# Performance work log

Hardware: AMD Instinct MI355X
Metric: run time of the kernel (lower is better)

The kernel has to match this reference:

```python
import jax, jax.numpy as jnp
import numpy as np

NEG_SLOPE = 0.2  # init arg negative_slope


def setup_inputs() -> dict:
    key = jax.random.key(0)
    k1, k2, k3, k4 = jax.random.split(key, 4)
    N, E, D_IN, D_OUT = 8192, 262144, 128, 128
    h = jax.random.normal(k1, (N, D_IN), dtype=jnp.float32)
    edge_index = jax.random.randint(k2, (2, E), 0, N, dtype=jnp.int64)
    # nn.Linear(in, out, bias=False) weight: [out, in]
    W = jax.random.normal(k3, (D_OUT, D_IN), dtype=jnp.float32) * (1.0 / np.sqrt(D_IN))
    # att parameter: [2*out, 1], xavier-uniform-ish scale
    lim = np.sqrt(6.0 / (2 * D_OUT + 1)) * 1.414
    att = jax.random.uniform(k4, (2 * D_OUT, 1), dtype=jnp.float32, minval=-lim, maxval=lim)
    return {"h": h, "edge_index": edge_index, "W": W, "att": att}


def reference(h, edge_index, W, att):
    # h: [N, d_in], edge_index: [2, E], W: [d_out, d_in], att: [2*d_out, 1]
    h_trans = h @ W.T                                  # [N, d_out]
    row, col = edge_index[0], edge_index[1]
    e = jnp.concatenate([h_trans[row], h_trans[col]], axis=1)  # [E, 2*d_out]
    edge_e = jnp.squeeze(e @ att, axis=-1)             # [E]
    edge_e = jnp.where(edge_e >= 0, edge_e, NEG_SLOPE * edge_e)  # leaky_relu
    N = h.shape[0]
    attention = jnp.zeros((N, N), dtype=h_trans.dtype).at[row, col].set(edge_e)
    attention = (attention + attention.T) * 0.5        # symmetrize
    fill_value = edge_e.max()                          # .item() -> constant (no grad)
    diag = jnp.arange(N)
    attention = attention.at[diag, diag].set(fill_value)
    attention = jax.nn.softmax(attention, axis=1)      # row softmax over dense NxN
    h_prime = attention @ h_trans                      # [N, d_out]
    h_prime = jax.nn.elu(h_prime)                      # concat=True -> ELU
    # F.dropout in eval mode is identity
    return h_prime, attention
```

## Files before the change

kernel.cpp:

```cpp
#include <hip/hip_runtime.h>
#include <stdint.h>

#define NN 8192
#define EE 262144
#define DD 128
#define NEGS 0.2f
#define HBITS 20

__device__ __forceinline__ unsigned f2ord(float f){
  unsigned u = __float_as_uint(f);
  return (u & 0x80000000u) ? ~u : (u | 0x80000000u);
}
__device__ __forceinline__ float ord2f(unsigned u){
  return __uint_as_float((u & 0x80000000u) ? (u & 0x7fffffffu) : ~u);
}
__device__ __forceinline__ unsigned hmix(int key){
  unsigned h = (unsigned)key * 2654435761u;
  h ^= h >> 15;
  return h;
}

__global__ void k_hashclear(int* hkeys, int* hvals){
  int i = blockIdx.x*256 + threadIdx.x;
  int4 m1 = {-1,-1,-1,-1};
  ((int4*)hkeys)[i] = m1;
  ((int4*)hvals)[i] = m1;
}

__global__ void k_init(int* cnt, int* cursor, float* T, unsigned* fillmax){
  int i = blockIdx.x*256 + threadIdx.x;
  if(i < NN){ cnt[i] = 0; cursor[i] = 0; }
  if(i < DD) T[i] = 0.f;
  if(i == 0) *fillmax = 0x007FFFFFu;
}

__global__ void k_wt(const float* __restrict__ W, float* __restrict__ wt){
  int idx = blockIdx.x*256 + threadIdx.x;
  int c = idx >> 7, k = idx & 127;
  wt[k*DD + c] = W[idx];
}

__global__ __launch_bounds__(256) void k_gemm(const float* __restrict__ h,
                                              const float* __restrict__ wt,
                                              float* __restrict__ ht){
  __shared__ float wl[64*DD];
  __shared__ float hl[16][132];
  int t = threadIdx.x;
  int row0 = blockIdx.x * 16;
  #pragma unroll
  for(int u=0;u<2;u++){
    int f4 = u*256 + t;
    int r = f4 >> 5, k4 = f4 & 31;
    float4 v = ((const float4*)(h + (size_t)(row0+r)*DD))[k4];
    *((float4*)&hl[r][k4*4]) = v;
  }
  int r  = t >> 4;
  int c0 = (t & 15) * 8;
  float acc[8];
  #pragma unroll
  for(int s=0;s<8;s++) acc[s]=0.f;
  for(int p=0;p<2;p++){
    __syncthreads();
    const float4* wsrc = (const float4*)(wt + p*64*DD);
    float4* wd = (float4*)wl;
    #pragma unroll
    for(int u=0;u<8;u++) wd[u*256+t] = wsrc[u*256+t];
    __syncthreads();
    #pragma unroll 4
    for(int kk=0;kk<64;kk++){
      float hv = hl[r][p*64+kk];
      const float* wrow = &wl[kk*DD + c0];
      #pragma unroll
      for(int s=0;s<8;s++) acc[s] += hv * wrow[s];
    }
  }
  float4 o0 = {acc[0],acc[1],acc[2],acc[3]};
  float4 o1 = {acc[4],acc[5],acc[6],acc[7]};
  float4* o = (float4*)(ht + (size_t)(row0+r)*DD + c0);
  o[0]=o0; o[1]=o1;
}

__global__ void k_colsum(const float* __restrict__ ht, float* T){
  __shared__ float part[256];
  int t = threadIdx.x; int c = t & 127; int half = t >> 7;
  float s = 0.f;
  int r0 = blockIdx.x*128 + half*64;
  for(int r=r0; r<r0+64; r++) s += ht[(size_t)r*DD + c];
  part[t] = s; __syncthreads();
  if(half==0) atomicAdd(&T[c], part[t] + part[t+128]);
}

__global__ void k_a(const float* __restrict__ ht, const float* __restrict__ att,
                    float* a1, float* a2){
  int lane = threadIdx.x & 63;
  int i = blockIdx.x*4 + (threadIdx.x >> 6);
  const float* hr = ht + (size_t)i*DD;
  float x1 = hr[lane]*att[lane]    + hr[lane+64]*att[lane+64];
  float x2 = hr[lane]*att[DD+lane] + hr[lane+64]*att[DD+lane+64];
  #pragma unroll
  for(int o=32;o>0;o>>=1){ x1 += __shfl_down(x1,o); x2 += __shfl_down(x2,o); }
  if(lane==0){ a1[i]=x1; a2[i]=x2; }
}

__global__ void k_edge(const int* __restrict__ ei, const float* __restrict__ a1,
                       const float* __restrict__ a2, float* __restrict__ val,
                       unsigned* fillmax, int* hkeys, int* hvals, int hmask){
  int k = blockIdx.x*256 + threadIdx.x;
  int r = ei[k], c = ei[EE + k];
  float e = a1[r] + a2[c];
  e = e >= 0.f ? e : NEGS*e;
  val[k] = e;
  float wm = e;
  #pragma unroll
  for(int o=32;o>0;o>>=1) wm = fmaxf(wm, __shfl_down(wm,o));
  __shared__ float sm[4];
  if((threadIdx.x & 63)==0) sm[threadIdx.x>>6] = wm;
  __syncthreads();
  if(threadIdx.x==0){
    float bm = fmaxf(fmaxf(sm[0],sm[1]), fmaxf(sm[2],sm[3]));
    atomicMax(fillmax, f2ord(bm));
  }
  if(r != c){
    int key = r*NN + c;
    unsigned slot = hmix(key) & hmask;
    while(true){
      int prev = atomicCAS(&hkeys[slot], -1, key);
      if(prev == -1 || prev == key){ atomicMax(&hvals[slot], k); break; }
      slot = (slot + 1) & hmask;
    }
  }
}

__global__ void k_count(const int* __restrict__ hkeys, int* cnt, int hmask){
  int s = blockIdx.x*256 + threadIdx.x;
  int key = hkeys[s];
  if(key < 0) return;
  int i = key >> 13, j = key & (NN-1);
  int rkey = j*NN + i;
  unsigned slot = hmix(rkey) & hmask;
  int found = 0;
  while(true){
    int kk = hkeys[slot];
    if(kk == rkey){ found = 1; break; }
    if(kk == -1) break;
    slot = (slot + 1) & hmask;
  }
  atomicAdd(&cnt[i], 1);
  if(!found) atomicAdd(&cnt[j], 1);
}

__global__ void k_scan(const int* __restrict__ cnt, int* rowstart){
  __shared__ int part[1024];
  int t = threadIdx.x;
  int loc[8]; int s = 0;
  #pragma unroll
  for(int u=0;u<8;u++){ loc[u]=s; s += cnt[t*8+u]; }
  part[t] = s; __syncthreads();
  for(int o=1;o<1024;o<<=1){
    int add = (t>=o) ? part[t-o] : 0;
    __syncthreads();
    part[t] += add;
    __syncthreads();
  }
  int pre = part[t] - s;
  #pragma unroll
  for(int u=0;u<8;u++) rowstart[t*8+u] = pre + loc[u];
  if(t==1023) rowstart[NN] = part[1023];
}

__global__ void k_fill(const int* __restrict__ hkeys, const int* __restrict__ hvals,
                       const float* __restrict__ val, const int* __restrict__ rowstart,
                       int* cursor, int* __restrict__ ecol, float* __restrict__ eval,
                       int hmask){
  int s = blockIdx.x*256 + threadIdx.x;
  int key = hkeys[s];
  if(key < 0) return;
  int i = key >> 13, j = key & (NN-1);
  int kwin = hvals[s];
  int rkey = j*NN + i;
  unsigned slot = hmix(rkey) & hmask;
  int krev = -1;
  while(true){
    int kk = hkeys[slot];
    if(kk == rkey){ krev = hvals[slot]; break; }
    if(kk == -1) break;
    slot = (slot + 1) & hmask;
  }
  float a = 0.5f * (val[kwin] + (krev >= 0 ? val[krev] : 0.f));
  int p = rowstart[i] + atomicAdd(&cursor[i], 1);
  ecol[p] = j; eval[p] = a;
  if(krev < 0){
    int q = rowstart[j] + atomicAdd(&cursor[j], 1);
    ecol[q] = i; eval[q] = a;
  }
}

__global__ __launch_bounds__(256) void k_row(const float* __restrict__ ht,
    const float* __restrict__ T, const int* __restrict__ rowst,
    const int* __restrict__ cnt, const int* __restrict__ ecol,
    const float* __restrict__ eval, const unsigned* __restrict__ fillmax,
    float* m_, float* inv_, float* z_, float* dg_, float* __restrict__ hprime){
  int lane = threadIdx.x & 63;
  int i = blockIdx.x*4 + (threadIdx.x >> 6);
  float fill = ord2f(*fillmax);
  int st = rowst[i], n = cnt[i];
  float mx = -INFINITY;
  for(int e=lane; e<n; e+=64) mx = fmaxf(mx, eval[st+e]);
  #pragma unroll
  for(int o=32;o>0;o>>=1) mx = fmaxf(mx, __shfl_xor(mx, o));
  float m = fmaxf(fill, mx);
  if(n < NN-1) m = fmaxf(m, 0.f);
  float dsum = 0.f;
  for(int e=lane; e<n; e+=64) dsum += __expf(eval[st+e]-m);
  #pragma unroll
  for(int o=32;o>0;o>>=1) dsum += __shfl_xor(dsum, o);
  float ez = __expf(-m);
  float ef = __expf(fill-m);
  float denom = dsum + ef + (float)(NN-1-n)*ez;
  float invd = 1.f/denom;
  if(lane==0){ m_[i]=m; inv_[i]=invd; z_[i]=ez*invd; dg_[i]=ef*invd; }
  const float* hti = ht + (size_t)i*DD;
  float acc0 = ez*T[lane]    + (ef-ez)*hti[lane];
  float acc1 = ez*T[lane+64] + (ef-ez)*hti[lane+64];
  for(int e=0;e<n;e++){
    int j = ecol[st+e];
    float w = __expf(eval[st+e]-m) - ez;
    const float* htj = ht + (size_t)j*DD;
    acc0 += w*htj[lane];
    acc1 += w*htj[lane+64];
  }
  acc0 *= invd; acc1 *= invd;
  acc0 = acc0 > 0.f ? acc0 : expm1f(acc0);
  acc1 = acc1 > 0.f ? acc1 : expm1f(acc1);
  hprime[(size_t)i*DD + lane]      = acc0;
  hprime[(size_t)i*DD + lane + 64] = acc1;
}

__global__ __launch_bounds__(256) void k_dense(const int* __restrict__ rowst,
    const int* __restrict__ cnt, const int* __restrict__ ecol,
    const float* __restrict__ eval, const float* __restrict__ m_,
    const float* __restrict__ inv_, const float* __restrict__ z_,
    const float* __restrict__ dg_, float* __restrict__ attn){
  __shared__ float rowbuf[NN];
  int i = blockIdx.x, t = threadIdx.x;
  float z = z_[i], m = m_[i], inv = inv_[i];
  float4 zv = {z,z,z,z};
  float4* rb4 = (float4*)rowbuf;
  #pragma unroll
  for(int u=0;u<8;u++) rb4[u*256+t] = zv;
  __syncthreads();
  int st = rowst[i], n = cnt[i];
  for(int e=t; e<n; e+=256)
    rowbuf[ecol[st+e]] = __expf(eval[st+e]-m)*inv;
  if(t==0) rowbuf[i] = dg_[i];
  __syncthreads();
  float4* o = (float4*)(attn + (size_t)i*NN);
  #pragma unroll
  for(int u=0;u<8;u++) o[u*256+t] = rb4[u*256+t];
}

extern "C" void kernel_launch(void* const* d_in, const int* in_sizes, int n_in,
                              void* d_out, int out_size, void* d_ws, size_t ws_size,
                              hipStream_t stream){
  const float* h   = (const float*)d_in[0];
  const int*   ei  = (const int*)d_in[1];
  const float* W   = (const float*)d_in[2];
  const float* att = (const float*)d_in[3];
  float* out = (float*)d_out;
  float* hprime = out;
  float* attn   = out + (size_t)NN*DD;

  const int hsize = 1 << HBITS, hmask = hsize - 1;
  int*   hkeys = (int*)attn;
  int*   hvals = hkeys + hsize;
  float* ht    = (float*)(hvals + hsize);
  float* val   = ht + (size_t)NN*DD;
  float* wt    = val + EE;
  float* a1    = wt + DD*DD;
  float* a2    = a1 + NN;

  char* ws = (char*)d_ws;
  size_t off = 0;
  auto alloc = [&](size_t bytes)->char*{
    char* p = ws + off;
    off = (off + bytes + 15) & ~(size_t)15;
    return p;
  };
  int*   ecol   = (int*)alloc((size_t)2*EE*4);
  float* eval   = (float*)alloc((size_t)2*EE*4);
  float* T      = (float*)alloc((size_t)DD*4);
  float* m_     = (float*)alloc((size_t)NN*4);
  float* inv_   = (float*)alloc((size_t)NN*4);
  float* z_     = (float*)alloc((size_t)NN*4);
  float* dg_    = (float*)alloc((size_t)NN*4);
  int*   cnt    = (int*)alloc((size_t)NN*4);
  int*   rowst  = (int*)alloc((size_t)(NN+1)*4);
  int*   cursor = (int*)alloc((size_t)NN*4);
  unsigned* fillmax = (unsigned*)alloc(16);

  k_hashclear<<<hsize/(256*4), 256, 0, stream>>>(hkeys, hvals);
  k_init  <<<32, 256, 0, stream>>>(cnt, cursor, T, fillmax);
  k_wt    <<<64, 256, 0, stream>>>(W, wt);
  k_gemm  <<<NN/16, 256, 0, stream>>>(h, wt, ht);
  k_colsum<<<64, 256, 0, stream>>>(ht, T);
  k_a     <<<NN/4, 256, 0, stream>>>(ht, att, a1, a2);
  k_edge  <<<EE/256, 256, 0, stream>>>(ei, a1, a2, val, fillmax, hkeys, hvals, hmask);
  k_count <<<hsize/256, 256, 0, stream>>>(hkeys, cnt, hmask);
  k_scan  <<<1, 1024, 0, stream>>>(cnt, rowst);
  k_fill  <<<hsize/256, 256, 0, stream>>>(hkeys, hvals, val, rowst, cursor, ecol, eval, hmask);
  k_row   <<<NN/4, 256, 0, stream>>>(ht, T, rowst, cnt, ecol, eval, fillmax, m_, inv_, z_, dg_, hprime);
  k_dense <<<NN, 256, 0, stream>>>(rowst, cnt, ecol, eval, m_, inv_, z_, dg_, attn);
}
```

Baseline: 229.0 us.

## Fuse setup, stats and output kernels; replace CSR build with fixed-capacity buckets

Merges the init/clear/transpose kernels into one setup kernel and the colsum and attention-score kernels into one stats kernel. Replaces the count, scan and fill CSR construction with per-row fixed-capacity buckets filled directly via atomics. Fuses the row-aggregation and dense attention-write kernels into a single per-row kernel using nontemporal stores, and remaps GEMM threads with float4 shared loads. This removes several launches and a pass over the hash table, but rows with more than the bucket capacity of neighbors would be silently truncated.

```diff
diff --git a/kernel.cpp b/kernel.cpp
--- a/kernel.cpp
+++ b/kernel.cpp
@@ -6,6 +6,11 @@
 #define DD 128
 #define NEGS 0.2f
 #define HBITS 20
+#define HSIZE (1<<HBITS)
+#define HMASK (HSIZE-1)
+#define BCAP 192
+
+typedef float f32x4 __attribute__((ext_vector_type(4)));
 
 __device__ __forceinline__ unsigned f2ord(float f){
   unsigned u = __float_as_uint(f);
@@ -20,24 +25,20 @@
   return h;
 }
 
-__global__ void k_hashclear(int* hkeys, int* hvals){
-  int i = blockIdx.x*256 + threadIdx.x;
+__global__ void k_setup(int* hkeys, int* hvals, int* cnt, float* T,
+                        unsigned* fillmax, const float* __restrict__ W,
+                        float* __restrict__ wt){
+  int gid = blockIdx.x*256 + threadIdx.x;
   int4 m1 = {-1,-1,-1,-1};
-  ((int4*)hkeys)[i] = m1;
-  ((int4*)hvals)[i] = m1;
-}
-
-__global__ void k_init(int* cnt, int* cursor, float* T, unsigned* fillmax){
-  int i = blockIdx.x*256 + threadIdx.x;
-  if(i < NN){ cnt[i] = 0; cursor[i] = 0; }
-  if(i < DD) T[i] = 0.f;
-  if(i == 0) *fillmax = 0x007FFFFFu;
-}
-
-__global__ void k_wt(const float* __restrict__ W, float* __restrict__ wt){
-  int idx = blockIdx.x*256 + threadIdx.x;
-  int c = idx >> 7, k = idx & 127;
-  wt[k*DD + c] = W[idx];
+  if(gid < HSIZE/4)            ((int4*)hkeys)[gid] = m1;
+  else if(gid < HSIZE/2)       ((int4*)hvals)[gid - HSIZE/4] = m1;
+  if(gid < NN/4)               ((int4*)cnt)[gid] = int4{0,0,0,0};
+  if(gid < DD/4)               ((float4*)T)[gid] = float4{0.f,0.f,0.f,0.f};
+  if(gid == 0)                 *fillmax = 0x007FFFFFu;
+  if(gid < DD*DD){
+    int c = gid >> 7, k = gid & 127;
+    wt[k*DD + c] = W[gid];
+  }
 }
 
 __global__ __launch_bounds__(256) void k_gemm(const float* __restrict__ h,
@@ -54,8 +55,8 @@
     float4 v = ((const float4*)(h + (size_t)(row0+r)*DD))[k4];
     *((float4*)&hl[r][k4*4]) = v;
   }
-  int r  = t >> 4;
-  int c0 = (t & 15) * 8;
+  int r  = t & 15;
+  int c0 = (t >> 4) * 8;
   float acc[8];
   #pragma unroll
   for(int s=0;s<8;s++) acc[s]=0.f;
@@ -66,45 +67,46 @@
     #pragma unroll
     for(int u=0;u<8;u++) wd[u*256+t] = wsrc[u*256+t];
     __syncthreads();
-    #pragma unroll 4
+    #pragma unroll 2
     for(int kk=0;kk<64;kk++){
       float hv = hl[r][p*64+kk];
-      const float* wrow = &wl[kk*DD + c0];
-      #pragma unroll
-      for(int s=0;s<8;s++) acc[s] += hv * wrow[s];
-    }
-  }
-  float4 o0 = {acc[0],acc[1],acc[2],acc[3]};
-  float4 o1 = {acc[4],acc[5],acc[6],acc[7]};
+      const float4* wr4 = (const float4*)&wl[kk*DD + c0];
+      float4 w0 = wr4[0], w1 = wr4[1];
+      acc[0] += hv*w0.x; acc[1] += hv*w0.y; acc[2] += hv*w0.z; acc[3] += hv*w0.w;
+      acc[4] += hv*w1.x; acc[5] += hv*w1.y; acc[6] += hv*w1.z; acc[7] += hv*w1.w;
+    }
+  }
   float4* o = (float4*)(ht + (size_t)(row0+r)*DD + c0);
-  o[0]=o0; o[1]=o1;
-}
-
-__global__ void k_colsum(const float* __restrict__ ht, float* T){
-  __shared__ float part[256];
-  int t = threadIdx.x; int c = t & 127; int half = t >> 7;
-  float s = 0.f;
-  int r0 = blockIdx.x*128 + half*64;
-  for(int r=r0; r<r0+64; r++) s += ht[(size_t)r*DD + c];
-  part[t] = s; __syncthreads();
-  if(half==0) atomicAdd(&T[c], part[t] + part[t+128]);
-}
-
-__global__ void k_a(const float* __restrict__ ht, const float* __restrict__ att,
-                    float* a1, float* a2){
-  int lane = threadIdx.x & 63;
-  int i = blockIdx.x*4 + (threadIdx.x >> 6);
+  o[0] = float4{acc[0],acc[1],acc[2],acc[3]};
+  o[1] = float4{acc[4],acc[5],acc[6],acc[7]};
+}
+
+__global__ __launch_bounds__(256) void k_stats(const float* __restrict__ ht,
+    const float* __restrict__ att, float* T, float* a1, float* a2){
+  int t = threadIdx.x, b = blockIdx.x;
+  int lane = t & 63;
+  int i = b*4 + (t >> 6);
   const float* hr = ht + (size_t)i*DD;
-  float x1 = hr[lane]*att[lane]    + hr[lane+64]*att[lane+64];
-  float x2 = hr[lane]*att[DD+lane] + hr[lane+64]*att[DD+lane+64];
+  float h0 = hr[lane], h1 = hr[lane+64];
+  float x1 = h0*att[lane]    + h1*att[lane+64];
+  float x2 = h0*att[DD+lane] + h1*att[DD+lane+64];
   #pragma unroll
   for(int o=32;o>0;o>>=1){ x1 += __shfl_down(x1,o); x2 += __shfl_down(x2,o); }
   if(lane==0){ a1[i]=x1; a2[i]=x2; }
+  if(b < 64){
+    __shared__ float part[256];
+    int c = t & 127, half = t >> 7;
+    float s = 0.f;
+    int r0 = b*128 + half*64;
+    for(int rr=r0; rr<r0+64; rr++) s += ht[(size_t)rr*DD + c];
+    part[t] = s; __syncthreads();
+    if(half==0) atomicAdd(&T[c], part[t] + part[t+128]);
+  }
 }
 
 __global__ void k_edge(const int* __restrict__ ei, const float* __restrict__ a1,
                        const float* __restrict__ a2, float* __restrict__ val,
-                       unsigned* fillmax, int* hkeys, int* hvals, int hmask){
+                       unsigned* fillmax, int* hkeys, int* hvals){
   int k = blockIdx.x*256 + threadIdx.x;
   int r = ei[k], c = ei[EE + k];
   float e = a1[r] + a2[c];
@@ -121,142 +123,108 @@
     atomicMax(fillmax, f2ord(bm));
   }
   if(r != c){
-    int key = r*NN + c;
-    unsigned slot = hmix(key) & hmask;
+    int key = (r<<13) | c;
+    unsigned slot = hmix(key) & HMASK;
     while(true){
       int prev = atomicCAS(&hkeys[slot], -1, key);
       if(prev == -1 || prev == key){ atomicMax(&hvals[slot], k); break; }
-      slot = (slot + 1) & hmask;
-    }
-  }
-}
-
-__global__ void k_count(const int* __restrict__ hkeys, int* cnt, int hmask){
-  int s = blockIdx.x*256 + threadIdx.x;
-  int key = hkeys[s];
-  if(key < 0) return;
-  int i = key >> 13, j = key & (NN-1);
-  int rkey = j*NN + i;
-  unsigned slot = hmix(rkey) & hmask;
-  int found = 0;
-  while(true){
-    int kk = hkeys[slot];
-    if(kk == rkey){ found = 1; break; }
-    if(kk == -1) break;
-    slot = (slot + 1) & hmask;
-  }
-  atomicAdd(&cnt[i], 1);
-  if(!found) atomicAdd(&cnt[j], 1);
-}
-
-__global__ void k_scan(const int* __restrict__ cnt, int* rowstart){
-  __shared__ int part[1024];
-  int t = threadIdx.x;
-  int loc[8]; int s = 0;
-  #pragma unroll
-  for(int u=0;u<8;u++){ loc[u]=s; s += cnt[t*8+u]; }
-  part[t] = s; __syncthreads();
-  for(int o=1;o<1024;o<<=1){
-    int add = (t>=o) ? part[t-o] : 0;
-    __syncthreads();
-    part[t] += add;
-    __syncthreads();
-  }
-  int pre = part[t] - s;
-  #pragma unroll
-  for(int u=0;u<8;u++) rowstart[t*8+u] = pre + loc[u];
-  if(t==1023) rowstart[NN] = part[1023];
+      slot = (slot + 1) & HMASK;
+    }
+  }
 }
 
 __global__ void k_fill(const int* __restrict__ hkeys, const int* __restrict__ hvals,
-                       const float* __restrict__ val, const int* __restrict__ rowstart,
-                       int* cursor, int* __restrict__ ecol, float* __restrict__ eval,
-                       int hmask){
-  int s = blockIdx.x*256 + threadIdx.x;
-  int key = hkeys[s];
-  if(key < 0) return;
-  int i = key >> 13, j = key & (NN-1);
-  int kwin = hvals[s];
-  int rkey = j*NN + i;
-  unsigned slot = hmix(rkey) & hmask;
-  int krev = -1;
-  while(true){
-    int kk = hkeys[slot];
-    if(kk == rkey){ krev = hvals[slot]; break; }
-    if(kk == -1) break;
-    slot = (slot + 1) & hmask;
-  }
-  float a = 0.5f * (val[kwin] + (krev >= 0 ? val[krev] : 0.f));
-  int p = rowstart[i] + atomicAdd(&cursor[i], 1);
-  ecol[p] = j; eval[p] = a;
-  if(krev < 0){
-    int q = rowstart[j] + atomicAdd(&cursor[j], 1);
-    ecol[q] = i; eval[q] = a;
-  }
-}
-
-__global__ __launch_bounds__(256) void k_row(const float* __restrict__ ht,
-    const float* __restrict__ T, const int* __restrict__ rowst,
-    const int* __restrict__ cnt, const int* __restrict__ ecol,
-    const float* __restrict__ eval, const unsigned* __restrict__ fillmax,
-    float* m_, float* inv_, float* z_, float* dg_, float* __restrict__ hprime){
-  int lane = threadIdx.x & 63;
-  int i = blockIdx.x*4 + (threadIdx.x >> 6);
+                       const float* __restrict__ val, int* cnt,
+                       int2* __restrict__ bucket){
+  int base = (blockIdx.x*256 + threadIdx.x) * 2;
+  #pragma unroll
+  for(int u=0;u<2;u++){
+    int s = base + u;
+    int key = hkeys[s];
+    if(key < 0) continue;
+    int i = key >> 13, j = key & (NN-1);
+    int kwin = hvals[s];
+    int rkey = (j<<13) | i;
+    unsigned slot = hmix(rkey) & HMASK;
+    int krev = -1;
+    while(true){
+      int kk = hkeys[slot];
+      if(kk == rkey){ krev = hvals[slot]; break; }
+      if(kk == -1) break;
+      slot = (slot + 1) & HMASK;
+    }
+    float a = 0.5f * (val[kwin] + (krev >= 0 ? val[krev] : 0.f));
+    int p = atomicAdd(&cnt[i], 1);
+    if(p < BCAP) bucket[(size_t)i*BCAP + p] = int2{j, __float_as_int(a)};
+    if(krev < 0){
+      int q = atomicAdd(&cnt[j], 1);
+      if(q < BCAP) bucket[(size_t)j*BCAP + q] = int2{i, __float_as_int(a)};
+    }
+  }
+}
+
+__global__ __launch_bounds__(256) void k_out(const float* __restrict__ ht,
+    const float* __restrict__ T, const int* __restrict__ cnt,
+    const int2* __restrict__ bucket, const unsigned* __restrict__ fillmax,
+    float* __restrict__ hprime, float* __restrict__ attn){
+  __shared__ float rowbuf[NN];
+  __shared__ float red[16];
+  __shared__ float hacc[2][DD];
+  int i = blockIdx.x, t = threadIdx.x;
+  int lane = t & 63, w = t >> 6;
   float fill = ord2f(*fillmax);
-  int st = rowst[i], n = cnt[i];
+  int n = min(cnt[i], BCAP);
+  const int2* brow = bucket + (size_t)i*BCAP;
   float mx = -INFINITY;
-  for(int e=lane; e<n; e+=64) mx = fmaxf(mx, eval[st+e]);
-  #pragma unroll
-  for(int o=32;o>0;o>>=1) mx = fmaxf(mx, __shfl_xor(mx, o));
+  for(int e=t; e<n; e+=256) mx = fmaxf(mx, __int_as_float(brow[e].y));
+  #pragma unroll
+  for(int o=32;o>0;o>>=1) mx = fmaxf(mx, __shfl_xor(mx,o));
+  if(lane==0) red[w] = mx;
+  __syncthreads();
+  mx = fmaxf(fmaxf(red[0],red[1]), fmaxf(red[2],red[3]));
   float m = fmaxf(fill, mx);
-  if(n < NN-1) m = fmaxf(m, 0.f);
-  float dsum = 0.f;
-  for(int e=lane; e<n; e+=64) dsum += __expf(eval[st+e]-m);
-  #pragma unroll
-  for(int o=32;o>0;o>>=1) dsum += __shfl_xor(dsum, o);
+  m = fmaxf(m, 0.f);
+  float ds = 0.f;
+  for(int e=t; e<n; e+=256) ds += __expf(__int_as_float(brow[e].y) - m);
+  #pragma unroll
+  for(int o=32;o>0;o>>=1) ds += __shfl_xor(ds,o);
+  if(lane==0) red[8+w] = ds;
+  __syncthreads();
+  ds = red[8]+red[9]+red[10]+red[11];
   float ez = __expf(-m);
-  float ef = __expf(fill-m);
-  float denom = dsum + ef + (float)(NN-1-n)*ez;
+  float ef = __expf(fill - m);
+  float denom = ds + ef + (float)(NN-1-n)*ez;
   float invd = 1.f/denom;
-  if(lane==0){ m_[i]=m; inv_[i]=invd; z_[i]=ez*invd; dg_[i]=ef*invd; }
-  const float* hti = ht + (size_t)i*DD;
-  float acc0 = ez*T[lane]    + (ef-ez)*hti[lane];
-  float acc1 = ez*T[lane+64] + (ef-ez)*hti[lane+64];
-  for(int e=0;e<n;e++){
-    int j = ecol[st+e];
-    float w = __expf(eval[st+e]-m) - ez;
-    const float* htj = ht + (size_t)j*DD;
-    acc0 += w*htj[lane];
-    acc1 += w*htj[lane+64];
-  }
-  acc0 *= invd; acc1 *= invd;
-  acc0 = acc0 > 0.f ? acc0 : expm1f(acc0);
-  acc1 = acc1 > 0.f ? acc1 : expm1f(acc1);
-  hprime[(size_t)i*DD + lane]      = acc0;
-  hprime[(size_t)i*DD + lane + 64] = acc1;
-}
-
-__global__ __launch_bounds__(256) void k_dense(const int* __restrict__ rowst,
-    const int* __restrict__ cnt, const int* __restrict__ ecol,
-    const float* __restrict__ eval, const float* __restrict__ m_,
-    const float* __restrict__ inv_, const float* __restrict__ z_,
-    const float* __restrict__ dg_, float* __restrict__ attn){
-  __shared__ float rowbuf[NN];
-  int i = blockIdx.x, t = threadIdx.x;
-  float z = z_[i], m = m_[i], inv = inv_[i];
+  int d = t & 127, half = t >> 7;
+  float acc = (half==0) ? (ez*T[d] + (ef-ez)*ht[(size_t)i*DD+d]) : 0.f;
+  for(int e=half; e<n; e+=2){
+    int2 be = brow[e];
+    float wgt = __expf(__int_as_float(be.y) - m) - ez;
+    acc += wgt * ht[(size_t)be.x*DD + d];
+  }
+  hacc[half][d] = acc;
+  __syncthreads();
+  if(t < DD){
+    float s = (hacc[0][t] + hacc[1][t]) * invd;
+    s = s > 0.f ? s : expm1f(s);
+    hprime[(size_t)i*DD + t] = s;
+  }
+  float z = ez*invd;
   float4 zv = {z,z,z,z};
   float4* rb4 = (float4*)rowbuf;
   #pragma unroll
   for(int u=0;u<8;u++) rb4[u*256+t] = zv;
   __syncthreads();
-  int st = rowst[i], n = cnt[i];
-  for(int e=t; e<n; e+=256)
-    rowbuf[ecol[st+e]] = __expf(eval[st+e]-m)*inv;
-  if(t==0) rowbuf[i] = dg_[i];
-  __syncthreads();
-  float4* o = (float4*)(attn + (size_t)i*NN);
-  #pragma unroll
-  for(int u=0;u<8;u++) o[u*256+t] = rb4[u*256+t];
+  for(int e=t; e<n; e+=256){
+    int2 be = brow[e];
+    rowbuf[be.x] = __expf(__int_as_float(be.y)-m)*invd;
+  }
+  if(t==0) rowbuf[i] = ef*invd;
+  __syncthreads();
+  const f32x4* rbn = (const f32x4*)rowbuf;
+  f32x4* o = (f32x4*)(attn + (size_t)i*NN);
+  #pragma unroll
+  for(int u=0;u<8;u++) __builtin_nontemporal_store(rbn[u*256+t], o + u*256+t);
 }
 
 extern "C" void kernel_launch(void* const* d_in, const int* in_sizes, int n_in,
@@ -270,44 +238,30 @@
   float* hprime = out;
   float* attn   = out + (size_t)NN*DD;
 
-  const int hsize = 1 << HBITS, hmask = hsize - 1;
   int*   hkeys = (int*)attn;
-  int*   hvals = hkeys + hsize;
-  float* ht    = (float*)(hvals + hsize);
-  float* val   = ht + (size_t)NN*DD;
-  float* wt    = val + EE;
-  float* a1    = wt + DD*DD;
+  int*   hvals = hkeys + HSIZE;
+  float* val   = (float*)(hvals + HSIZE);
+  float* a1    = val + EE;
   float* a2    = a1 + NN;
 
   char* ws = (char*)d_ws;
   size_t off = 0;
   auto alloc = [&](size_t bytes)->char*{
     char* p = ws + off;
-    off = (off + bytes + 15) & ~(size_t)15;
+    off = (off + bytes + 255) & ~(size_t)255;
     return p;
   };
-  int*   ecol   = (int*)alloc((size_t)2*EE*4);
-  float* eval   = (float*)alloc((size_t)2*EE*4);
-  float* T      = (float*)alloc((size_t)DD*4);
-  float* m_     = (float*)alloc((size_t)NN*4);
-  float* inv_   = (float*)alloc((size_t)NN*4);
-  float* z_     = (float*)alloc((size_t)NN*4);
-  float* dg_    = (float*)alloc((size_t)NN*4);
-  int*   cnt    = (int*)alloc((size_t)NN*4);
-  int*   rowst  = (int*)alloc((size_t)(NN+1)*4);
-  int*   cursor = (int*)alloc((size_t)NN*4);
-  unsigned* fillmax = (unsigned*)alloc(16);
-
-  k_hashclear<<<hsize/(256*4), 256, 0, stream>>>(hkeys, hvals);
-  k_init  <<<32, 256, 0, stream>>>(cnt, cursor, T, fillmax);
-  k_wt    <<<64, 256, 0, stream>>>(W, wt);
+  float* ht      = (float*)alloc((size_t)NN*DD*4);
+  float* wt      = (float*)alloc((size_t)DD*DD*4);
+  float* T       = (float*)alloc((size_t)DD*4);
+  int*   cnt     = (int*)alloc((size_t)NN*4);
+  unsigned* fillmax = (unsigned*)alloc(256);
+  int2*  bucket  = (int2*)alloc((size_t)NN*BCAP*8);
+
+  k_setup <<<2048, 256, 0, stream>>>(hkeys, hvals, cnt, T, fillmax, W, wt);
   k_gemm  <<<NN/16, 256, 0, stream>>>(h, wt, ht);
-  k_colsum<<<64, 256, 0, stream>>>(ht, T);
-  k_a     <<<NN/4, 256, 0, stream>>>(ht, att, a1, a2);
-  k_edge  <<<EE/256, 256, 0, stream>>>(ei, a1, a2, val, fillmax, hkeys, hvals, hmask);
-  k_count <<<hsize/256, 256, 0, stream>>>(hkeys, cnt, hmask);
-  k_scan  <<<1, 1024, 0, stream>>>(cnt, rowst);
-  k_fill  <<<hsize/256, 256, 0, stream>>>(hkeys, hvals, val, rowst, cursor, ecol, eval, hmask);
-  k_row   <<<NN/4, 256, 0, stream>>>(ht, T, rowst, cnt, ecol, eval, fillmax, m_, inv_, z_, dg_, hprime);
-  k_dense <<<NN, 256, 0, stream>>>(rowst, cnt, ecol, eval, m_, inv_, z_, dg_, attn);
-}
+  k_stats <<<NN/4, 256, 0, stream>>>(ht, att, T, a1, a2);
+  k_edge  <<<EE/256, 256, 0, stream>>>(ei, a1, a2, val, fillmax, hkeys, hvals);
+  k_fill  <<<HSIZE/512, 256, 0, stream>>>(hkeys, hvals, val, cnt, bucket);
+  k_out   <<<NN, 256, 0, stream>>>(ht, T, cnt, bucket, fillmax, hprime, attn);
+}
```

Result: slower. 235.4 us (+2.8%).
